# Optimization experiments

Hardware: AMD Instinct MI355X
Metric: run time of the kernel (lower is better)

The kernel has to match this reference:

```python
import jax, jax.numpy as jnp
import numpy as np

H = 16
D_MODEL = 1024
D_K = D_MODEL // H
L = 4096


def setup_inputs() -> dict:
    key = jax.random.key(0)
    ks = jax.random.split(key, 11)
    s = 1.0 / np.sqrt(D_MODEL)
    inp = {
        "query": jax.random.normal(ks[0], (L, D_MODEL), dtype=jnp.float32),
        "key": jax.random.normal(ks[1], (L, D_MODEL), dtype=jnp.float32),
        "value": jax.random.normal(ks[2], (L, D_MODEL), dtype=jnp.float32),
        "Wq": jax.random.uniform(ks[3], (D_MODEL, D_MODEL), jnp.float32, -s, s),
        "Wk": jax.random.uniform(ks[4], (D_MODEL, D_MODEL), jnp.float32, -s, s),
        "Wv": jax.random.uniform(ks[5], (D_MODEL, D_MODEL), jnp.float32, -s, s),
        "Wo": jax.random.uniform(ks[6], (D_MODEL, D_MODEL), jnp.float32, -s, s),
        "bq": jax.random.uniform(ks[7], (D_MODEL,), jnp.float32, -s, s),
        "bk": jax.random.uniform(ks[8], (D_MODEL,), jnp.float32, -s, s),
        "bv": jax.random.uniform(ks[9], (D_MODEL,), jnp.float32, -s, s),
        "bo": jax.random.uniform(ks[10], (D_MODEL,), jnp.float32, -s, s),
    }
    return inp


def reference(query, key, value, Wq, Wk, Wv, Wo, bq, bk, bv, bo):
    # projections: torch Linear computes x @ W.T + b
    def proj(x, W, b):
        # [L, d_model] -> [h, L, d_k]
        y = x @ W.T + b
        return y.reshape(L, H, D_K).transpose(1, 0, 2)

    q = proj(query, Wq, bq)   # [h, L, d_k]
    k = proj(key, Wk, bk)
    v = proj(value, Wv, bv)

    scores = jnp.einsum("hqd,hkd->hqk", q, k) / jnp.sqrt(jnp.float32(D_K))  # [h, L, L]
    p = jax.nn.softmax(scores, axis=-1)
    x = jnp.einsum("hqk,hkd->hqd", p, v)         # [h, L, d_k]
    x = x.transpose(1, 0, 2).reshape(L, H * D_K)  # [L, d_model]
    return x @ Wo.T + bo
```

## Files before the change

kernel.cpp:

```cpp
#include <hip/hip_runtime.h>

#define L_SEQ 4096
#define DM 1024
#define NH 16
#define DK 64

typedef short s16x8 __attribute__((ext_vector_type(8)));
typedef float f32x4 __attribute__((ext_vector_type(4)));
typedef float f32x16 __attribute__((ext_vector_type(16)));
typedef unsigned u32x2 __attribute__((ext_vector_type(2)));
typedef unsigned short u16t;
typedef unsigned int u32t;

typedef __attribute__((address_space(1))) unsigned int as1_u32;
typedef __attribute__((address_space(3))) unsigned int as3_u32;

#define GLOAD_LDS16(gsrc, ldst) \
  __builtin_amdgcn_global_load_lds((as1_u32*)(gsrc), (as3_u32*)(ldst), 16, 0, 0)

__device__ __forceinline__ u16t f2bf(float f) {
  union { float f; unsigned u; } v; v.f = f;
  unsigned u = v.u;
  u += 0x7fffu + ((u >> 16) & 1u);
  return (u16t)(u >> 16);
}

__device__ __forceinline__ float fexp2(float x) {
  float r;
  asm("v_exp_f32 %0, %1" : "=v"(r) : "v"(x));
  return r;
}

__device__ __forceinline__ float max3f(float a, float b, float c) {
  return fmaxf(fmaxf(a, b), c);
}

__device__ __forceinline__ float bflo(u32t u) {
  union { u32t u; float f; } v; v.u = u << 16; return v.f;
}
__device__ __forceinline__ float bfhi(u32t u) {
  union { u32t u; float f; } v; v.u = u & 0xffff0000u; return v.f;
}

struct CvtArgs { const float* s[7]; u16t* d[7]; };

__global__ __launch_bounds__(256) void cvt_all(CvtArgs a) {
  int g = blockIdx.x * 256 + threadIdx.x;
  int seg, off;
  if (g < 1572864) { seg = g >> 19;               off = g & 524287; }
  else             { int t = g - 1572864; seg = 3 + (t >> 17); off = t & 131071; }
  const float* src = a.s[seg] + (size_t)off * 8;
  u16t* dst = a.d[seg] + (size_t)off * 8;
  float4 x = *(const float4*)(src);
  float4 y = *(const float4*)(src + 4);
  uint4 o;
  o.x = (u32t)f2bf(x.x) | ((u32t)f2bf(x.y) << 16);
  o.y = (u32t)f2bf(x.z) | ((u32t)f2bf(x.w) << 16);
  o.z = (u32t)f2bf(y.x) | ((u32t)f2bf(y.y) << 16);
  o.w = (u32t)f2bf(y.z) | ((u32t)f2bf(y.w) << 16);
  *(uint4*)dst = o;
}

struct QkvArgs {
  const u16t* A[3]; const u16t* Bm[3]; const float* bias[3]; u16t* C[3];
  float scale0;
};

__global__ __launch_bounds__(256)
void gemm_qkv(QkvArgs ga) {
  __shared__ unsigned char lds[2][2][8192];
  const int bid = blockIdx.x;
  const int z = bid >> 8;
  const int b = bid & 255;
  const int bc = (z == 2) ? (b & 31) : (b & 7);
  const int br = (z == 2) ? (b >> 5) : (b >> 3);
  const int N  = (z == 2) ? L_SEQ : DM;
  const float osc = (z == 0) ? ga.scale0 : 1.0f;
  const bool rowb = (z == 2);
  const u16t* A = ga.A[z];
  const u16t* Bm = ga.Bm[z];
  const float* bias = ga.bias[z];
  u16t* C = ga.C[z];
  const int K = DM;

  const int tid = threadIdx.x;
  const int lane = tid & 63;
  const int wv = tid >> 6;
  const int wr = wv >> 1, wc = wv & 1;
  const int l15 = lane & 15, l4 = lane >> 4;

  const int r_st = tid >> 2;
  const int c_st = (tid & 3) ^ ((r_st >> 1) & 3);
  const u16t* a0 = A + (size_t)(br * 128 + r_st) * K + c_st * 8;
  const u16t* a1 = a0 + (size_t)64 * K;
  const u16t* b0 = Bm + (size_t)(bc * 128 + r_st) * K + c_st * 8;
  const u16t* b1 = b0 + (size_t)64 * K;
  const int woff = wv * 1024;

  f32x4 acc[4][4] = {};

  auto stage = [&](int buf, int k0) {
    GLOAD_LDS16(a0 + k0, &lds[buf][0][woff]);
    GLOAD_LDS16(a1 + k0, &lds[buf][0][4096 + woff]);
    GLOAD_LDS16(b0 + k0, &lds[buf][1][woff]);
    GLOAD_LDS16(b1 + k0, &lds[buf][1][4096 + woff]);
  };

  const int nt = K >> 5;
  stage(0, 0);
  int buf = 0;
  for (int t = 0; t < nt; ++t) {
    __syncthreads();
    if (t + 1 < nt) stage(buf ^ 1, (t + 1) * 32);
    s16x8 af[4], bfr[4];
    #pragma unroll
    for (int m = 0; m < 4; ++m) {
      int r = wr * 64 + m * 16 + l15;
      int sl = l4 ^ ((r >> 1) & 3);
      af[m] = *(const s16x8*)&lds[buf][0][r * 64 + (sl << 4)];
    }
    #pragma unroll
    for (int n = 0; n < 4; ++n) {
      int r = wc * 64 + n * 16 + l15;
      int sl = l4 ^ ((r >> 1) & 3);
      bfr[n] = *(const s16x8*)&lds[buf][1][r * 64 + (sl << 4)];
    }
    #pragma unroll
    for (int m = 0; m < 4; ++m)
      #pragma unroll
      for (int n = 0; n < 4; ++n)
        acc[m][n] = __builtin_amdgcn_mfma_f32_16x16x32_bf16(af[m], bfr[n], acc[m][n], 0, 0, 0);
    buf ^= 1;
  }

  #pragma unroll
  for (int m = 0; m < 4; ++m) {
    #pragma unroll
    for (int n = 0; n < 4; ++n) {
      #pragma unroll
      for (int i = 0; i < 4; ++i) {
        int row = br * 128 + wr * 64 + m * 16 + l4 * 4 + i;
        int col = bc * 128 + wc * 64 + n * 16 + l15;
        float v = (acc[m][n][i] + (rowb ? bias[row] : bias[col])) * osc;
        C[(size_t)row * N + col] = f2bf(v);
      }
    }
  }
}

__global__ __launch_bounds__(256)
void gemm_out(const u16t* __restrict__ A, const u16t* __restrict__ B,
              const float* __restrict__ bias, float* __restrict__ C,
              int M, int N, int K) {
  __shared__ unsigned char lds[2][12288];
  const int tid = threadIdx.x;
  const int lane = tid & 63;
  const int wv = tid >> 6;
  const int wr = wv >> 1, wc = wv & 1;
  const int l15 = lane & 15, l4 = lane >> 4;
  const int bc = blockIdx.x, br = blockIdx.y;

  const int r_st = tid >> 2;
  const int c_st = (tid & 3) ^ ((r_st >> 1) & 3);
  const u16t* a0 = A + (size_t)(br * 128 + r_st) * K + c_st * 8;
  const u16t* a1 = a0 + (size_t)64 * K;
  const u16t* b0 = B + (size_t)(bc * 64 + r_st) * K + c_st * 8;
  const int woff = wv * 1024;

  f32x4 acc[4][2] = {};

  auto stage = [&](int buf, int k0) {
    GLOAD_LDS16(a0 + k0, &lds[buf][woff]);
    GLOAD_LDS16(a1 + k0, &lds[buf][4096 + woff]);
    GLOAD_LDS16(b0 + k0, &lds[buf][8192 + woff]);
  };

  const int nt = K >> 5;
  stage(0, 0);
  int buf = 0;
  for (int t = 0; t < nt; ++t) {
    __syncthreads();
    if (t + 1 < nt) stage(buf ^ 1, (t + 1) * 32);
    s16x8 af[4], bfr[2];
    #pragma unroll
    for (int m = 0; m < 4; ++m) {
      int r = wr * 64 + m * 16 + l15;
      int sl = l4 ^ ((r >> 1) & 3);
      af[m] = *(const s16x8*)&lds[buf][r * 64 + (sl << 4)];
    }
    #pragma unroll
    for (int n = 0; n < 2; ++n) {
      int r = wc * 32 + n * 16 + l15;
      int sl = l4 ^ ((r >> 1) & 3);
      bfr[n] = *(const s16x8*)&lds[buf][8192 + r * 64 + (sl << 4)];
    }
    #pragma unroll
    for (int m = 0; m < 4; ++m)
      #pragma unroll
      for (int n = 0; n < 2; ++n)
        acc[m][n] = __builtin_amdgcn_mfma_f32_16x16x32_bf16(af[m], bfr[n], acc[m][n], 0, 0, 0);
    buf ^= 1;
  }

  #pragma unroll
  for (int m = 0; m < 4; ++m) {
    #pragma unroll
    for (int n = 0; n < 2; ++n) {
      #pragma unroll
      for (int i = 0; i < 4; ++i) {
        int row = br * 128 + wr * 64 + m * 16 + l4 * 4 + i;
        int col = bc * 64 + wc * 32 + n * 16 + l15;
        C[(size_t)row * N + col] = acc[m][n][i] + bias[col];
      }
    }
  }
}

#define PKBF(dst, a, b) \
  asm("v_cvt_pk_bf16_f32 %0, %1, %2" : "=v"(dst) : "v"(a), "v"(b))

#define MAKE_FRAG(S, B, FR) { \
    u32t w0, w1, w2, w3; \
    PKBF(w0, S[B + 0], S[B + 1]); PKBF(w1, S[B + 2], S[B + 3]); \
    PKBF(w2, S[B + 4], S[B + 5]); PKBF(w3, S[B + 6], S[B + 7]); \
    u32x2 r02 = __builtin_amdgcn_permlane32_swap(w0, w2, false, false); \
    u32x2 r13 = __builtin_amdgcn_permlane32_swap(w1, w3, false, false); \
    union { u32t u[4]; s16x8 v; } uu; \
    uu.u[0] = r02[0]; uu.u[1] = r13[0]; uu.u[2] = r02[1]; uu.u[3] = r13[1]; \
    FR = uu.v; }

__global__ __launch_bounds__(512, 4)
void attn_fused(const u16t* __restrict__ Qp, const u16t* __restrict__ Kp,
                const u16t* __restrict__ VpT, u16t* __restrict__ Op0,
                u16t* __restrict__ Op1, float2* __restrict__ Ml0,
                float2* __restrict__ Ml1) {
  __shared__ unsigned char sStage[3][16384];

  const int tid = threadIdx.x;
  const int lane = tid & 63;
  const int w = tid >> 6;
  const int l31 = lane & 31;
  const int hi = lane >> 5;
  const int h = blockIdx.y;
  const int z = blockIdx.z;
  const int kvbase = z * (L_SEQ / 2);
  const int qrow = blockIdx.x * 256 + w * 32 + l31;
  u16t* Opz = z ? Op1 : Op0;
  float2* Mlz = z ? Ml1 : Ml0;

  s16x8 qf[4];
  {
    const u16t* qsrc = Qp + (size_t)qrow * DM + h * DK + hi * 8;
    #pragma unroll
    for (int c = 0; c < 4; ++c) qf[c] = *(const s16x8*)(qsrc + c * 16);
  }

  f32x16 acc0 = {}, acc1 = {};
  float mrow = -3.0e38f, lrow = 0.f;

  auto stage = [&](int buf, int kv) {
    GLOAD_LDS16(Kp + (size_t)(kv + lane) * DM + h * DK + w * 8,
                &sStage[buf][w * 1024]);
    GLOAD_LDS16(VpT + (size_t)(h * DK + lane) * L_SEQ + kv + w * 8,
                &sStage[buf][8192 + w * 1024]);
  };

  auto compute = [&](const unsigned char* sb) {
    f32x16 st0 = {}, st1 = {};
    __builtin_amdgcn_s_setprio(1);
    #pragma unroll
    for (int c = 0; c < 4; ++c) {
      const unsigned char* kp = sb + (((c * 2 + hi) << 10));
      s16x8 kf0 = *(const s16x8*)(kp + (l31 << 4));
      s16x8 kf1 = *(const s16x8*)(kp + ((32 + l31) << 4));
      st0 = __builtin_amdgcn_mfma_f32_32x32x16_bf16(kf0, qf[c], st0, 0, 0, 0);
      st1 = __builtin_amdgcn_mfma_f32_32x32x16_bf16(kf1, qf[c], st1, 0, 0, 0);
    }
    __builtin_amdgcn_s_setprio(0);

    float v0 = max3f(st0[0], st0[1], st0[2]);
    float v1 = max3f(st0[3], st0[4], st0[5]);
    float v2 = max3f(st0[6], st0[7], st0[8]);
    float v3 = max3f(st0[9], st0[10], st0[11]);
    float v4 = max3f(st0[12], st0[13], st0[14]);
    float v5 = max3f(st1[0], st1[1], st1[2]);
    float v6 = max3f(st1[3], st1[4], st1[5]);
    float v7 = max3f(st1[6], st1[7], st1[8]);
    float v8 = max3f(st1[9], st1[10], st1[11]);
    float v9 = max3f(st1[12], st1[13], st1[14]);
    float va = fmaxf(st0[15], st1[15]);
    float mx = max3f(max3f(v0, v1, v2), max3f(v3, v4, v5),
                     max3f(max3f(v6, v7, v8), v9, va));
    mx = fmaxf(mx, __shfl_xor(mx, 32));

    float mnew = fmaxf(mrow, mx);
    if (!__all(mx <= mrow)) {
      float alpha = fexp2(mrow - mnew);
      lrow *= alpha;
      #pragma unroll
      for (int r = 0; r < 16; ++r) { acc0[r] *= alpha; acc1[r] *= alpha; }
      mrow = mnew;
    }
    const float m2 = mrow;

    #pragma unroll
    for (int r = 0; r < 16; ++r) {
      st0[r] = fexp2(st0[r] - m2);
      st1[r] = fexp2(st1[r] - m2);
    }
    float s8[8];
    #pragma unroll
    for (int r = 0; r < 8; ++r)
      s8[r] = (st0[2*r] + st0[2*r+1]) + (st1[2*r] + st1[2*r+1]);
    float rs = ((s8[0] + s8[1]) + (s8[2] + s8[3])) +
               ((s8[4] + s8[5]) + (s8[6] + s8[7]));
    rs += __shfl_xor(rs, 32);
    lrow += rs;

    __builtin_amdgcn_s_setprio(1);
    #pragma unroll
    for (int cc = 0; cc < 4; ++cc) {
      s16x8 pfr;
      if (cc == 0)      MAKE_FRAG(st0, 0, pfr)
      else if (cc == 1) MAKE_FRAG(st0, 8, pfr)
      else if (cc == 2) MAKE_FRAG(st1, 0, pfr)
      else              MAKE_FRAG(st1, 8, pfr)
      const unsigned char* vp = sb + 8192 + ((cc * 2 + hi) << 10);
      s16x8 vf0 = *(const s16x8*)(vp + (l31 << 4));
      s16x8 vf1 = *(const s16x8*)(vp + ((32 + l31) << 4));
      acc0 = __builtin_amdgcn_mfma_f32_32x32x16_bf16(vf0, pfr, acc0, 0, 0, 0);
      acc1 = __builtin_amdgcn_mfma_f32_32x32x16_bf16(vf1, pfr, acc1, 0, 0, 0);
    }
    __builtin_amdgcn_s_setprio(0);
  };

  stage(0, kvbase);
  stage(1, kvbase + 64);
  int cur = 0, nstage = 2;
  for (int t = 0; t < 31; ++t) {
    asm volatile("s_waitcnt vmcnt(2)" ::: "memory");
    __builtin_amdgcn_s_barrier();
    __builtin_amdgcn_sched_barrier(0);
    if (t < 30) {
      stage(nstage, kvbase + (t + 2) * 64);
      nstage = (nstage == 2) ? 0 : nstage + 1;
    }
    compute(sStage[cur]);
    cur = (cur == 2) ? 0 : cur + 1;
  }
  asm volatile("s_waitcnt vmcnt(0)" ::: "memory");
  __builtin_amdgcn_s_barrier();
  __builtin_amdgcn_sched_barrier(0);
  compute(sStage[cur]);

  u16t* orow = Opz + (size_t)qrow * DM + h * DK;
  #pragma unroll
  for (int rq = 0; rq < 4; ++rq) {
    union { u16t h4[4]; uint2 v; } p0, p1;
    #pragma unroll
    for (int i = 0; i < 4; ++i) {
      p0.h4[i] = f2bf(acc0[4 * rq + i]);
      p1.h4[i] = f2bf(acc1[4 * rq + i]);
    }
    int d0 = 8 * rq + 4 * hi;
    *(uint2*)(orow + d0)      = p0.v;
    *(uint2*)(orow + 32 + d0) = p1.v;
  }
  if (hi == 0) Mlz[h * L_SEQ + qrow] = make_float2(mrow, lrow);
}

__global__ __launch_bounds__(256)
void attn_combine(const u16t* __restrict__ O0, const u16t* __restrict__ O1,
                  const float2* __restrict__ Ml0, const float2* __restrict__ Ml1,
                  u16t* __restrict__ AO) {
  int g = blockIdx.x * 256 + threadIdx.x;
  int qh = g >> 2;
  int d0 = (g & 3) * 16;
  int q = qh >> 4, h = qh & 15;
  size_t off = (size_t)q * DM + h * DK + d0;

  float2 ml0 = Ml0[h * L_SEQ + q];
  float2 ml1 = Ml1[h * L_SEQ + q];
  float m = fmaxf(ml0.x, ml1.x);
  float w0 = fexp2(ml0.x - m), w1 = fexp2(ml1.x - m);
  float inv = 1.0f / (ml0.y * w0 + ml1.y * w1);
  float s0 = w0 * inv, s1 = w1 * inv;

  uint4 a[2], b[2], o[2];
  a[0] = *(const uint4*)(O0 + off);     a[1] = *(const uint4*)(O0 + off + 8);
  b[0] = *(const uint4*)(O1 + off);     b[1] = *(const uint4*)(O1 + off + 8);
  #pragma unroll
  for (int k = 0; k < 2; ++k) {
    u32t* au = (u32t*)&a[k]; u32t* bu = (u32t*)&b[k]; u32t* ou = (u32t*)&o[k];
    #pragma unroll
    for (int j = 0; j < 4; ++j) {
      float lo = bflo(au[j]) * s0 + bflo(bu[j]) * s1;
      float hf = bfhi(au[j]) * s0 + bfhi(bu[j]) * s1;
      ou[j] = (u32t)f2bf(lo) | ((u32t)f2bf(hf) << 16);
    }
  }
  *(uint4*)(AO + off)     = o[0];
  *(uint4*)(AO + off + 8) = o[1];
}

extern "C" void kernel_launch(void* const* d_in, const int* in_sizes, int n_in,
                              void* d_out, int out_size, void* d_ws, size_t ws_size,
                              hipStream_t stream) {
  const float* query = (const float*)d_in[0];
  const float* key_  = (const float*)d_in[1];
  const float* value = (const float*)d_in[2];
  const float* Wq = (const float*)d_in[3];
  const float* Wk = (const float*)d_in[4];
  const float* Wv = (const float*)d_in[5];
  const float* Wo = (const float*)d_in[6];
  const float* bq = (const float*)d_in[7];
  const float* bk = (const float*)d_in[8];
  const float* bv = (const float*)d_in[9];
  const float* bo = (const float*)d_in[10];

  char* ws = (char*)d_ws;
  const size_t MB = 1u << 20;
  u16t* qb  = (u16t*)(ws + 0 * MB);
  u16t* kb  = (u16t*)(ws + 8 * MB);
  u16t* vb  = (u16t*)(ws + 16 * MB);
  u16t* wqb = (u16t*)(ws + 24 * MB);
  u16t* wkb = (u16t*)(ws + 26 * MB);
  u16t* wvb = (u16t*)(ws + 28 * MB);
  u16t* wob = (u16t*)(ws + 30 * MB);
  u16t* Qp  = (u16t*)(ws + 32 * MB);
  u16t* Kp  = (u16t*)(ws + 40 * MB);
  u16t* VpT = (u16t*)(ws + 48 * MB);
  u16t* AO  = (u16t*)(ws + 56 * MB);

  u16t* Op0   = (u16t*)(ws + 0 * MB);
  u16t* Op1   = (u16t*)(ws + 8 * MB);
  float2* Ml0 = (float2*)(ws + 16 * MB);
  float2* Ml1 = (float2*)(ws + 17 * MB);

  const float QSCALE = 0.125f * 1.4426950408889634f;

  CvtArgs ca;
  ca.s[0] = query; ca.s[1] = key_; ca.s[2] = value;
  ca.s[3] = Wq; ca.s[4] = Wk; ca.s[5] = Wv; ca.s[6] = Wo;
  ca.d[0] = qb; ca.d[1] = kb; ca.d[2] = vb;
  ca.d[3] = wqb; ca.d[4] = wkb; ca.d[5] = wvb; ca.d[6] = wob;
  cvt_all<<<dim3(8192), dim3(256), 0, stream>>>(ca);

  QkvArgs ga;
  ga.A[0] = qb;  ga.Bm[0] = wqb; ga.bias[0] = bq; ga.C[0] = Qp;
  ga.A[1] = kb;  ga.Bm[1] = wkb; ga.bias[1] = bk; ga.C[1] = Kp;
  ga.A[2] = wvb; ga.Bm[2] = vb;  ga.bias[2] = bv; ga.C[2] = VpT;
  ga.scale0 = QSCALE;
  gemm_qkv<<<dim3(768), dim3(256), 0, stream>>>(ga);

  attn_fused<<<dim3(L_SEQ / 256, NH, 2), dim3(512), 0, stream>>>(
      Qp, Kp, VpT, Op0, Op1, Ml0, Ml1);

  attn_combine<<<dim3(1024), dim3(256), 0, stream>>>(Op0, Op1, Ml0, Ml1, AO);

  gemm_out<<<dim3(DM / 64, L_SEQ / 128), dim3(256), 0, stream>>>(
      AO, wob, bo, (float*)d_out, L_SEQ, DM, DM);
}
```

Measured before the change: 169.4 us.

## Widen output GEMM tile, unroll attention pipeline, add lazy softmax rescale

The output projection GEMM now uses 128x128 tiles instead of 128x64, with each wave computing 4x4 MFMA tiles, which raises operand reuse and halves the grid. The attention kernel drops per-iteration buffer index arithmetic: it advances K/V pointers incrementally, precomputes LDS read offsets, and unrolls the triple-buffer ring into a fixed phase sequence. The online softmax now rescales only when the running max grows by more than 8 (log2 units), which skips most rescale passes but lets exponentials reach up to 2^8 before renormalisation. It also vectorises the subtract and reduction code.

```diff
diff --git a/kernel.cpp b/kernel.cpp
--- a/kernel.cpp
+++ b/kernel.cpp
@@ -7,6 +7,7 @@
 
 typedef short s16x8 __attribute__((ext_vector_type(8)));
 typedef float f32x4 __attribute__((ext_vector_type(4)));
+typedef float f32x8 __attribute__((ext_vector_type(8)));
 typedef float f32x16 __attribute__((ext_vector_type(16)));
 typedef unsigned u32x2 __attribute__((ext_vector_type(2)));
 typedef unsigned short u16t;
@@ -152,7 +153,7 @@
 void gemm_out(const u16t* __restrict__ A, const u16t* __restrict__ B,
               const float* __restrict__ bias, float* __restrict__ C,
               int M, int N, int K) {
-  __shared__ unsigned char lds[2][12288];
+  __shared__ unsigned char lds[2][2][8192];
   const int tid = threadIdx.x;
   const int lane = tid & 63;
   const int wv = tid >> 6;
@@ -164,15 +165,17 @@
   const int c_st = (tid & 3) ^ ((r_st >> 1) & 3);
   const u16t* a0 = A + (size_t)(br * 128 + r_st) * K + c_st * 8;
   const u16t* a1 = a0 + (size_t)64 * K;
-  const u16t* b0 = B + (size_t)(bc * 64 + r_st) * K + c_st * 8;
+  const u16t* b0 = B + (size_t)(bc * 128 + r_st) * K + c_st * 8;
+  const u16t* b1 = b0 + (size_t)64 * K;
   const int woff = wv * 1024;
 
-  f32x4 acc[4][2] = {};
+  f32x4 acc[4][4] = {};
 
   auto stage = [&](int buf, int k0) {
-    GLOAD_LDS16(a0 + k0, &lds[buf][woff]);
-    GLOAD_LDS16(a1 + k0, &lds[buf][4096 + woff]);
-    GLOAD_LDS16(b0 + k0, &lds[buf][8192 + woff]);
+    GLOAD_LDS16(a0 + k0, &lds[buf][0][woff]);
+    GLOAD_LDS16(a1 + k0, &lds[buf][0][4096 + woff]);
+    GLOAD_LDS16(b0 + k0, &lds[buf][1][woff]);
+    GLOAD_LDS16(b1 + k0, &lds[buf][1][4096 + woff]);
   };
 
   const int nt = K >> 5;
@@ -181,23 +184,23 @@
   for (int t = 0; t < nt; ++t) {
     __syncthreads();
     if (t + 1 < nt) stage(buf ^ 1, (t + 1) * 32);
-    s16x8 af[4], bfr[2];
+    s16x8 af[4], bfr[4];
     #pragma unroll
     for (int m = 0; m < 4; ++m) {
       int r = wr * 64 + m * 16 + l15;
       int sl = l4 ^ ((r >> 1) & 3);
-      af[m] = *(const s16x8*)&lds[buf][r * 64 + (sl << 4)];
-    }
-    #pragma unroll
-    for (int n = 0; n < 2; ++n) {
-      int r = wc * 32 + n * 16 + l15;
+      af[m] = *(const s16x8*)&lds[buf][0][r * 64 + (sl << 4)];
+    }
+    #pragma unroll
+    for (int n = 0; n < 4; ++n) {
+      int r = wc * 64 + n * 16 + l15;
       int sl = l4 ^ ((r >> 1) & 3);
-      bfr[n] = *(const s16x8*)&lds[buf][8192 + r * 64 + (sl << 4)];
+      bfr[n] = *(const s16x8*)&lds[buf][1][r * 64 + (sl << 4)];
     }
     #pragma unroll
     for (int m = 0; m < 4; ++m)
       #pragma unroll
-      for (int n = 0; n < 2; ++n)
+      for (int n = 0; n < 4; ++n)
         acc[m][n] = __builtin_amdgcn_mfma_f32_16x16x32_bf16(af[m], bfr[n], acc[m][n], 0, 0, 0);
     buf ^= 1;
   }
@@ -205,11 +208,11 @@
   #pragma unroll
   for (int m = 0; m < 4; ++m) {
     #pragma unroll
-    for (int n = 0; n < 2; ++n) {
+    for (int n = 0; n < 4; ++n) {
       #pragma unroll
       for (int i = 0; i < 4; ++i) {
         int row = br * 128 + wr * 64 + m * 16 + l4 * 4 + i;
-        int col = bc * 64 + wc * 32 + n * 16 + l15;
+        int col = bc * 128 + wc * 64 + n * 16 + l15;
         C[(size_t)row * N + col] = acc[m][n][i] + bias[col];
       }
     }
@@ -258,21 +261,26 @@
   f32x16 acc0 = {}, acc1 = {};
   float mrow = -3.0e38f, lrow = 0.f;
 
-  auto stage = [&](int buf, int kv) {
-    GLOAD_LDS16(Kp + (size_t)(kv + lane) * DM + h * DK + w * 8,
-                &sStage[buf][w * 1024]);
-    GLOAD_LDS16(VpT + (size_t)(h * DK + lane) * L_SEQ + kv + w * 8,
-                &sStage[buf][8192 + w * 1024]);
+  const u16t* kptr = Kp + (size_t)(kvbase + lane) * DM + h * DK + w * 8;
+  const u16t* vptr = VpT + (size_t)(h * DK + lane) * L_SEQ + kvbase + w * 8;
+  const int woffK = w * 1024;
+
+  auto stage = [&](int buf) {
+    GLOAD_LDS16(kptr, &sStage[buf][woffK]);
+    GLOAD_LDS16(vptr, &sStage[buf][8192 + woffK]);
+    kptr += 64 * DM;
+    vptr += 64;
   };
+
+  const int rdoff = (hi << 10) + (l31 << 4);
 
   auto compute = [&](const unsigned char* sb) {
     f32x16 st0 = {}, st1 = {};
     __builtin_amdgcn_s_setprio(1);
     #pragma unroll
     for (int c = 0; c < 4; ++c) {
-      const unsigned char* kp = sb + (((c * 2 + hi) << 10));
-      s16x8 kf0 = *(const s16x8*)(kp + (l31 << 4));
-      s16x8 kf1 = *(const s16x8*)(kp + ((32 + l31) << 4));
+      s16x8 kf0 = *(const s16x8*)(sb + c * 2048);
+      s16x8 kf1 = *(const s16x8*)(sb + c * 2048 + 512);
       st0 = __builtin_amdgcn_mfma_f32_32x32x16_bf16(kf0, qf[c], st0, 0, 0, 0);
       st1 = __builtin_amdgcn_mfma_f32_32x32x16_bf16(kf1, qf[c], st1, 0, 0, 0);
     }
@@ -293,27 +301,28 @@
                      max3f(max3f(v6, v7, v8), v9, va));
     mx = fmaxf(mx, __shfl_xor(mx, 32));
 
-    float mnew = fmaxf(mrow, mx);
-    if (!__all(mx <= mrow)) {
+    if (!__all(mx <= mrow + 8.0f)) {
+      float mnew = fmaxf(mrow, mx);
       float alpha = fexp2(mrow - mnew);
       lrow *= alpha;
-      #pragma unroll
-      for (int r = 0; r < 16; ++r) { acc0[r] *= alpha; acc1[r] *= alpha; }
+      acc0 *= alpha;
+      acc1 *= alpha;
       mrow = mnew;
     }
-    const float m2 = mrow;
-
+
+    st0 = st0 - mrow;
+    st1 = st1 - mrow;
     #pragma unroll
     for (int r = 0; r < 16; ++r) {
-      st0[r] = fexp2(st0[r] - m2);
-      st1[r] = fexp2(st1[r] - m2);
-    }
-    float s8[8];
-    #pragma unroll
-    for (int r = 0; r < 8; ++r)
-      s8[r] = (st0[2*r] + st0[2*r+1]) + (st1[2*r] + st1[2*r+1]);
-    float rs = ((s8[0] + s8[1]) + (s8[2] + s8[3])) +
-               ((s8[4] + s8[5]) + (s8[6] + s8[7]));
+      st0[r] = fexp2(st0[r]);
+      st1[r] = fexp2(st1[r]);
+    }
+    f32x16 sv = st0 + st1;
+    f32x8 s8v = __builtin_shufflevector(sv, sv, 0, 1, 2, 3, 4, 5, 6, 7) +
+                __builtin_shufflevector(sv, sv, 8, 9, 10, 11, 12, 13, 14, 15);
+    f32x4 s4v = __builtin_shufflevector(s8v, s8v, 0, 1, 2, 3) +
+                __builtin_shufflevector(s8v, s8v, 4, 5, 6, 7);
+    float rs = (s4v[0] + s4v[1]) + (s4v[2] + s4v[3]);
     rs += __shfl_xor(rs, 32);
     lrow += rs;
 
@@ -325,33 +334,38 @@
       else if (cc == 1) MAKE_FRAG(st0, 8, pfr)
       else if (cc == 2) MAKE_FRAG(st1, 0, pfr)
       else              MAKE_FRAG(st1, 8, pfr)
-      const unsigned char* vp = sb + 8192 + ((cc * 2 + hi) << 10);
-      s16x8 vf0 = *(const s16x8*)(vp + (l31 << 4));
-      s16x8 vf1 = *(const s16x8*)(vp + ((32 + l31) << 4));
+      s16x8 vf0 = *(const s16x8*)(sb + 8192 + cc * 2048);
+      s16x8 vf1 = *(const s16x8*)(sb + 8192 + cc * 2048 + 512);
       acc0 = __builtin_amdgcn_mfma_f32_32x32x16_bf16(vf0, pfr, acc0, 0, 0, 0);
       acc1 = __builtin_amdgcn_mfma_f32_32x32x16_bf16(vf1, pfr, acc1, 0, 0, 0);
     }
     __builtin_amdgcn_s_setprio(0);
   };
 
-  stage(0, kvbase);
-  stage(1, kvbase + 64);
-  int cur = 0, nstage = 2;
-  for (int t = 0; t < 31; ++t) {
+  auto phase = [&](int bc, int bs) {
     asm volatile("s_waitcnt vmcnt(2)" ::: "memory");
     __builtin_amdgcn_s_barrier();
     __builtin_amdgcn_sched_barrier(0);
-    if (t < 30) {
-      stage(nstage, kvbase + (t + 2) * 64);
-      nstage = (nstage == 2) ? 0 : nstage + 1;
-    }
-    compute(sStage[cur]);
-    cur = (cur == 2) ? 0 : cur + 1;
-  }
+    stage(bs);
+    compute(sStage[bc] + rdoff);
+  };
+
+  stage(0);
+  stage(1);
+  #pragma unroll 1
+  for (int c = 0; c < 10; ++c) {
+    phase(0, 2);
+    phase(1, 0);
+    phase(2, 1);
+  }
+  asm volatile("s_waitcnt vmcnt(2)" ::: "memory");
+  __builtin_amdgcn_s_barrier();
+  __builtin_amdgcn_sched_barrier(0);
+  compute(sStage[0] + rdoff);
   asm volatile("s_waitcnt vmcnt(0)" ::: "memory");
   __builtin_amdgcn_s_barrier();
   __builtin_amdgcn_sched_barrier(0);
-  compute(sStage[cur]);
+  compute(sStage[1] + rdoff);
 
   u16t* orow = Opz + (size_t)qrow * DM + h * DK;
   #pragma unroll
@@ -458,6 +472,6 @@
 
   attn_combine<<<dim3(1024), dim3(256), 0, stream>>>(Op0, Op1, Ml0, Ml1, AO);
 
-  gemm_out<<<dim3(DM / 64, L_SEQ / 128), dim3(256), 0, stream>>>(
+  gemm_out<<<dim3(DM / 128, L_SEQ / 128), dim3(256), 0, stream>>>(
       AO, wob, bo, (float*)d_out, L_SEQ, DM, DM);
 }
```

Result: faster. 165.8 us (-2.2%).
